# Kernel tuning notes

Measured on AMD Instinct MI355X. Metric: run time of the kernel, lower is better.

The kernel has to match this reference:

```python
import jax, jax.numpy as jnp
import numpy as np

STATE_DIM = 128
ACT_DIM = 32
ENC_K = 10   # encoder_spine_dim
DEC_K = 10   # decoder_dim
H0, H1 = 2048, 2048
BATCH = 16384
MAX_ACTION = 1.0
STD0 = 0.3872983346207417  # sqrt(0.15)


def setup_inputs() -> dict:
    key = jax.random.key(0)
    ks = jax.random.split(key, 10)
    state = jax.random.normal(ks[0], (BATCH, STATE_DIM), dtype=jnp.float32)
    # encoder params: mean linspace over mean_range, std constant
    mean_enc = jnp.broadcast_to(jnp.linspace(-3.0, 3.0, ENC_K, dtype=jnp.float32),
                                (1, STATE_DIM, ENC_K))
    std_enc = jnp.full((1, STATE_DIM, ENC_K), STD0, dtype=jnp.float32)
    def lin(k, fan_in, fan_out):
        bound = 1.0 / np.sqrt(fan_in)
        k1, k2 = jax.random.split(k)
        W = jax.random.uniform(k1, (fan_out, fan_in), jnp.float32, -bound, bound)
        b = jax.random.uniform(k2, (fan_out,), jnp.float32, -bound, bound)
        return W, b
    W1, b1 = lin(ks[1], STATE_DIM * ENC_K, H0)
    W2, b2 = lin(ks[2], H0, H1)
    W3, b3 = lin(ks[3], H1, ACT_DIM * DEC_K)
    # grouped conv1d: weight [act_dim, 1, dec_k], bias [act_dim]
    bound = 1.0 / np.sqrt(DEC_K)
    Wd = jax.random.uniform(ks[4], (ACT_DIM, 1, DEC_K), jnp.float32, -bound, bound)
    bd = jax.random.uniform(ks[5], (ACT_DIM,), jnp.float32, -bound, bound)
    return {"state": state, "mean_enc": mean_enc, "std_enc": std_enc,
            "W1": W1, "b1": b1, "W2": W2, "b2": b2, "W3": W3, "b3": b3,
            "Wd": Wd, "bd": bd}


def reference(state, mean_enc, std_enc, W1, b1, W2, b2, W3, b3, Wd, bd):
    # Population-coding encoder: sigmoid((obs - mean)/std), flattened
    spine = jax.nn.sigmoid((state[:, :, None] - mean_enc) / std_enc)  # [B, D, K]
    spine = spine.reshape(state.shape[0], -1)                         # [B, D*K]
    a = jax.nn.relu(spine @ W1.T + b1)
    a = jax.nn.relu(a @ W2.T + b2)
    a = a @ W3.T + b3                                                 # [B, A*Kd]
    d = a.reshape(-1, ACT_DIM, DEC_K)                                 # [B, A, Kd]
    # grouped Conv1d with kernel == length => per-channel dot product
    raw = jnp.einsum('bak,ak->ba', d, Wd[:, 0, :]) + bd               # [B, A]
    return MAX_ACTION * jnp.tanh(raw)
```

## Files before the change

### kernel.cpp

```cpp
#include <hip/hip_runtime.h>
#include <hip/hip_bf16.h>
#include <stdint.h>

#define BATCH   16384
#define SDIM    128
#define ENCK    10
#define ADIM    32
#define DECK    10
#define HID     2048
#define KSPINE  1280

typedef __bf16 bf16x8 __attribute__((ext_vector_type(8)));
typedef float  f32x4  __attribute__((ext_vector_type(4)));

typedef __attribute__((address_space(1))) const void kGlobalVoid;
typedef __attribute__((address_space(3))) void       kLdsVoid;

__device__ __forceinline__ unsigned short f2b(float f) {
  union { float f; unsigned u; } v; v.f = f;
  unsigned r = v.u + 0x7fffu + ((v.u >> 16) & 1u);
  return (unsigned short)(r >> 16);
}

__global__ void f2b_kernel(const float* __restrict__ in, unsigned* __restrict__ out, int n2) {
  int i = blockIdx.x * blockDim.x + threadIdx.x;
  if (i >= n2) return;
  float2 v = reinterpret_cast<const float2*>(in)[i];
  out[i] = (unsigned)f2b(v.x) | ((unsigned)f2b(v.y) << 16);
}

__global__ void encoder_kernel(const float* __restrict__ state,
                               const float* __restrict__ mean,
                               const float* __restrict__ stdv,
                               unsigned* __restrict__ spine) {
  int idx = blockIdx.x * blockDim.x + threadIdx.x;
  if (idx >= BATCH * SDIM) return;
  int d = idx & (SDIM - 1);
  float x = state[idx];
  float vals[ENCK];
#pragma unroll
  for (int k = 0; k < ENCK; ++k) {
    float z = (x - mean[d * ENCK + k]) / stdv[d * ENCK + k];
    vals[k] = 1.f / (1.f + __expf(-z));
  }
  unsigned* dst = spine + idx * (ENCK / 2);
#pragma unroll
  for (int k = 0; k < ENCK / 2; ++k)
    dst[k] = (unsigned)f2b(vals[2 * k]) | ((unsigned)f2b(vals[2 * k + 1]) << 16);
}

__global__ void weff_kernel(const float* __restrict__ W3, const float* __restrict__ Wd,
                            unsigned short* __restrict__ Weff) {
  int idx = blockIdx.x * 256 + threadIdx.x;
  int a = idx >> 11, j = idx & 2047;
  float s = 0.f;
#pragma unroll
  for (int k = 0; k < DECK; ++k)
    s += Wd[a * DECK + k] * W3[(size_t)(a * DECK + k) * HID + j];
  Weff[idx] = f2b(s);
}

__global__ void beff_kernel(const float* __restrict__ b3, const float* __restrict__ Wd,
                            const float* __restrict__ bd, float* __restrict__ beff) {
  int a = threadIdx.x;
  if (a >= ADIM) return;
  float s = bd[a];
#pragma unroll
  for (int k = 0; k < DECK; ++k) s += Wd[a * DECK + k] * b3[a * DECK + k];
  beff[a] = s;
}


#define A0B 0
#define B0B 32768
#define A1B 65536
#define B1B 98304

#define FENCE asm volatile("" ::: "memory")

#define STAGE(BASEPTR, R0A, R0B, LDS0, LDS1, KT)                                             \
  __builtin_amdgcn_global_load_lds((kGlobalVoid*)((BASEPTR) + (size_t)((R0A) + rs) * K + (KT) + ce), \
                                   (kLdsVoid*)(smem + (LDS0) + t * 16), 16, 0, 0);           \
  __builtin_amdgcn_global_load_lds((kGlobalVoid*)((BASEPTR) + (size_t)((R0B) + rs) * K + (KT) + ce), \
                                   (kLdsVoid*)(smem + (LDS1) + t * 16), 16, 0, 0);

#define DS_AF(DST, ABASE, MPN)                                                               \
  _Pragma("unroll")                                                                          \
  for (int j2 = 0; j2 < 2; ++j2) {                                                           \
    _Pragma("unroll")                                                                        \
    for (int ks = 0; ks < 2; ++ks) {                                                         \
      int rowl = wr * 128 + (MPN) * 32 + j2 * 16 + lr;                                       \
      DST[j2][ks] = *reinterpret_cast<const bf16x8*>(                                        \
          smem + (ABASE) + rowl * 128 + ((((ks) << 6) | (kh << 4)) ^ swz));                  \
    }                                                                                        \
  }

#define DS_B2(DST, NP, BBASE)                                                                \
  _Pragma("unroll")                                                                          \
  for (int ks = 0; ks < 2; ++ks) {                                                           \
    int rowl = wc * 64 + (NP) * 16 + lr;                                                     \
    DST[NP][ks] = *reinterpret_cast<const bf16x8*>(                                          \
        smem + (BBASE) + rowl * 128 + ((((ks) << 6) | (kh << 4)) ^ swz));                    \
  }

#define DS_BF(DST, BBASE)                                                                    \
  _Pragma("unroll")                                                                          \
  for (int n = 0; n < 4; ++n) {                                                              \
    _Pragma("unroll")                                                                        \
    for (int ks = 0; ks < 2; ++ks) {                                                         \
      int rowl = wc * 64 + n * 16 + lr;                                                      \
      DST[n][ks] = *reinterpret_cast<const bf16x8*>(                                         \
          smem + (BBASE) + rowl * 128 + ((((ks) << 6) | (kh << 4)) ^ swz));                  \
    }                                                                                        \
  }

#define MFMA16(MP, AF, BF)                                                                   \
  _Pragma("unroll")                                                                          \
  for (int j2 = 0; j2 < 2; ++j2)                                                             \
    _Pragma("unroll")                                                                        \
    for (int n = 0; n < 4; ++n)                                                              \
      _Pragma("unroll")                                                                      \
      for (int ks = 0; ks < 2; ++ks)                                                         \
        acc[(MP) * 2 + j2][n] = __builtin_amdgcn_mfma_f32_16x16x32_bf16(                     \
            AF[j2][ks], BF[n][ks], acc[(MP) * 2 + j2][n], 0, 0, 0);

#define SGB_PHASE                                                                            \
  __builtin_amdgcn_sched_group_barrier(0x8, 2, 0);                                           \
  __builtin_amdgcn_sched_group_barrier(0x100, 1, 0);                                         \
  __builtin_amdgcn_sched_group_barrier(0x8, 2, 0);                                           \
  __builtin_amdgcn_sched_group_barrier(0x100, 1, 0);                                         \
  __builtin_amdgcn_sched_group_barrier(0x20, 2, 0);                                          \
  __builtin_amdgcn_sched_group_barrier(0x8, 3, 0);                                           \
  __builtin_amdgcn_sched_group_barrier(0x100, 1, 0);                                         \
  __builtin_amdgcn_sched_group_barrier(0x8, 3, 0);                                           \
  __builtin_amdgcn_sched_group_barrier(0x100, 1, 0);                                         \
  __builtin_amdgcn_sched_group_barrier(0x8, 3, 0);                                           \
  __builtin_amdgcn_sched_group_barrier(0x100, 1, 0);                                         \
  __builtin_amdgcn_sched_group_barrier(0x8, 3, 0);                                           \
  __builtin_amdgcn_sched_group_barrier(0x100, 1, 0);

#define VM_NONE
#define VM2 asm volatile("s_waitcnt vmcnt(2)" ::: "memory"); __builtin_amdgcn_sched_barrier(0);
#define VM6 asm volatile("s_waitcnt vmcnt(6)" ::: "memory"); __builtin_amdgcn_sched_barrier(0);

#define PH(MP, AF_C, AF_N, BF_C, BF_N, NXT_A, NXT_MP, BBASE_N, VMW, STG)                     \
  do {                                                                                       \
    asm volatile("s_waitcnt lgkmcnt(0)" ::: "memory");                                       \
    __builtin_amdgcn_sched_barrier(0);                                                       \
    VMW                                                                                      \
    __builtin_amdgcn_s_setprio(1);                                                           \
    MFMA16(MP, AF_C, BF_C);                                                                  \
    __builtin_amdgcn_s_setprio(0);                                                           \
    DS_AF(AF_N, NXT_A, NXT_MP);                                                              \
    DS_B2(BF_N, MP, BBASE_N);                                                                \
    STG;                                                                                     \
    SGB_PHASE;                                                                               \
    FENCE;                                                                                   \
    __builtin_amdgcn_s_barrier();                                                            \
  } while (0)

__global__ __launch_bounds__(512, 2) void gemm256(
    const unsigned short* __restrict__ A,
    const unsigned short* __restrict__ Bw,
    const float* __restrict__ bias,
    unsigned short* __restrict__ Cout,
    int K, int NI) {
  __shared__ char smem[131072];

  const int t    = threadIdx.x;
  const int lane = t & 63;
  const int w    = t >> 6;
  const int wr   = w >> 2;
  const int wc   = w & 3;
  const int lr   = lane & 15;
  const int kh   = lane >> 4;
  const int swz  = (lr & 7) << 4;
  const int rs   = t >> 3;
  const int ce   = ((t & 7) ^ (rs & 7)) << 3;

  const int bid = blockIdx.x;
  const int xcd = bid & 7, idx = bid >> 3;
  const int row0 = (xcd * 8 + (idx >> 3)) * 256;
  const int col0 = (idx & 7) * 256;

  f32x4 acc[8][4];
#pragma unroll
  for (int m = 0; m < 8; ++m)
#pragma unroll
    for (int n = 0; n < 4; ++n)
      acc[m][n] = (f32x4){0.f, 0.f, 0.f, 0.f};

  bf16x8 afc[2][2], afn[2][2], bfA[4][2], bfB[4][2];

  STAGE(Bw, col0 + 0,   col0 + 64,  B0B + 0,     B0B + 8192,  0);
  STAGE(Bw, col0 + 128, col0 + 192, B0B + 16384, B0B + 24576, 0);
  STAGE(A,  row0 + 0,   row0 + 128, A0B + 0,     A0B + 16384, 0);
  STAGE(A,  row0 + 64,  row0 + 192, A0B + 8192,  A0B + 24576, 0);
  STAGE(Bw, col0 + 0,   col0 + 64,  B1B + 0,     B1B + 8192,  64);
  STAGE(Bw, col0 + 128, col0 + 192, B1B + 16384, B1B + 24576, 64);
  STAGE(A,  row0 + 0,   row0 + 128, A1B + 0,     A1B + 16384, 64);
  asm volatile("s_waitcnt vmcnt(0)" ::: "memory");
  FENCE;
  __builtin_amdgcn_s_barrier();
  DS_AF(afc, A0B, 0);
  DS_BF(bfA, B0B);

  for (int i = 0; i < NI; ++i) {
    int kt0 = i << 7;
    int kt1 = kt0 + 64;
    int kt2 = kt0 + 128; if (kt2 >= K) kt2 -= K;
    int kt3 = kt0 + 192; if (kt3 >= K) kt3 -= K;

    PH(0, afc, afn, bfA, bfB, A0B, 1, B1B, VM2,
       STAGE(A,  row0 + 64,  row0 + 192, A1B + 8192,  A1B + 24576, kt1));
    PH(1, afn, afc, bfA, bfB, A0B, 2, B1B, VM_NONE,
       STAGE(Bw, col0 + 0,   col0 + 64,  B0B + 0,     B0B + 8192,  kt2));
    PH(2, afc, afn, bfA, bfB, A0B, 3, B1B, VM_NONE,
       STAGE(Bw, col0 + 128, col0 + 192, B0B + 16384, B0B + 24576, kt2));
    PH(3, afn, afc, bfA, bfB, A1B, 0, B1B, VM6,
       STAGE(A,  row0 + 0,   row0 + 128, A0B + 0,     A0B + 16384, kt2));
    PH(0, afc, afn, bfB, bfA, A1B, 1, B0B, VM2,
       STAGE(A,  row0 + 64,  row0 + 192, A0B + 8192,  A0B + 24576, kt2));
    PH(1, afn, afc, bfB, bfA, A1B, 2, B0B, VM_NONE,
       STAGE(Bw, col0 + 0,   col0 + 64,  B1B + 0,     B1B + 8192,  kt3));
    PH(2, afc, afn, bfB, bfA, A1B, 3, B0B, VM_NONE,
       STAGE(Bw, col0 + 128, col0 + 192, B1B + 16384, B1B + 24576, kt3));
    PH(3, afn, afc, bfB, bfA, A0B, 0, B0B, VM6,
       STAGE(A,  row0 + 0,   row0 + 128, A1B + 0,     A1B + 16384, kt3));
  }

#pragma unroll
  for (int m = 0; m < 8; ++m) {
    int gr0 = row0 + wr * 128 + m * 16 + kh * 4;
#pragma unroll
    for (int n = 0; n < 4; ++n) {
      int gc = col0 + wc * 64 + n * 16 + lr;
      float bv = bias[gc];
#pragma unroll
      for (int v = 0; v < 4; ++v) {
        float val = fmaxf(acc[m][n][v] + bv, 0.f);
        Cout[(size_t)(gr0 + v) * 2048 + gc] = f2b(val);
      }
    }
  }
}

__global__ __launch_bounds__(128) void gemm_skinny(
    const unsigned short* __restrict__ A,
    const unsigned short* __restrict__ Bw,
    const float* __restrict__ beff,
    float* __restrict__ out) {
  const int t = threadIdx.x, lane = t & 63, w = t >> 6;
  const int lr = lane & 15, kh = lane >> 4;
  const int row0 = (blockIdx.x * 2 + w) * 16;
  f32x4 acc[2];
  acc[0] = (f32x4){0.f, 0.f, 0.f, 0.f};
  acc[1] = (f32x4){0.f, 0.f, 0.f, 0.f};

  const unsigned short* Arow = A  + (size_t)(row0 + lr) * HID + kh * 8;
  const unsigned short* B0   = Bw + (size_t)(lr) * HID + kh * 8;
  const unsigned short* B1   = Bw + (size_t)(16 + lr) * HID + kh * 8;

#pragma unroll 4
  for (int kt = 0; kt < HID; kt += 32) {
    bf16x8 a  = *reinterpret_cast<const bf16x8*>(Arow + kt);
    bf16x8 b0 = *reinterpret_cast<const bf16x8*>(B0 + kt);
    bf16x8 b1 = *reinterpret_cast<const bf16x8*>(B1 + kt);
    acc[0] = __builtin_amdgcn_mfma_f32_16x16x32_bf16(a, b0, acc[0], 0, 0, 0);
    acc[1] = __builtin_amdgcn_mfma_f32_16x16x32_bf16(a, b1, acc[1], 0, 0, 0);
  }
#pragma unroll
  for (int n = 0; n < 2; ++n)
#pragma unroll
    for (int v = 0; v < 4; ++v) {
      int row = row0 + kh * 4 + v;
      int col = n * 16 + lr;
      out[(size_t)row * ADIM + col] = tanhf(acc[n][v] + beff[col]);
    }
}

extern "C" void kernel_launch(void* const* d_in, const int* in_sizes, int n_in,
                              void* d_out, int out_size, void* d_ws, size_t ws_size,
                              hipStream_t stream) {
  const float* state    = (const float*)d_in[0];
  const float* mean_enc = (const float*)d_in[1];
  const float* std_enc  = (const float*)d_in[2];
  const float* W1 = (const float*)d_in[3];
  const float* b1 = (const float*)d_in[4];
  const float* W2 = (const float*)d_in[5];
  const float* b2 = (const float*)d_in[6];
  const float* W3 = (const float*)d_in[7];
  const float* b3 = (const float*)d_in[8];
  const float* Wd = (const float*)d_in[9];
  const float* bd = (const float*)d_in[10];

  char* ws = (char*)d_ws;
  unsigned short* W1b   = (unsigned short*)(ws + 0);
  unsigned short* W2b   = (unsigned short*)(ws + 5242880);
  unsigned short* Weff  = (unsigned short*)(ws + 13631488);
  float*          beff  = (float*)(ws + 13762560);
  unsigned short* spine = (unsigned short*)(ws + 13762688);
  unsigned short* h1    = (unsigned short*)(ws + 55705728);
  unsigned short* h2    = (unsigned short*)(ws + 122814592);

  f2b_kernel<<<5120, 256, 0, stream>>>(W1, (unsigned*)W1b, 1310720);
  f2b_kernel<<<8192, 256, 0, stream>>>(W2, (unsigned*)W2b, 2097152);
  weff_kernel<<<256, 256, 0, stream>>>(W3, Wd, Weff);
  beff_kernel<<<1, 64, 0, stream>>>(b3, Wd, bd, beff);

  encoder_kernel<<<(BATCH * SDIM) / 256, 256, 0, stream>>>(state, mean_enc, std_enc, (unsigned*)spine);

  gemm256<<<512, 512, 0, stream>>>(spine, W1b, b1, h1, KSPINE, KSPINE / 128);
  gemm256<<<512, 512, 0, stream>>>(h1,    W2b, b2, h2, HID,    HID / 128);
  gemm_skinny<<<BATCH / 32, 128, 0, stream>>>(h2, Weff, beff, (float*)d_out);
}
```

Before: 249.1 us.

## Split skinny GEMM K across four waves and widen encoder parallelism

The final skinny GEMM now gives each 16-row tile its own block of four waves. Each wave covers a quarter of the K dimension, and the partial results are reduced through shared memory. The encoder is also remapped so each thread writes one packed pair of sigmoid outputs instead of all ten, which spreads the writes over five times as many threads and coalesces the stores. Both changes aim to raise parallelism and memory efficiency in small kernels. They add an LDS reduction, a barrier, and recomputed state loads.

Result: no change. 249.9 us (+0.3%).

```diff
diff --git a/kernel.cpp b/kernel.cpp
--- a/kernel.cpp
+++ b/kernel.cpp
@@ -29,24 +29,21 @@
   out[i] = (unsigned)f2b(v.x) | ((unsigned)f2b(v.y) << 16);
 }
 
-__global__ void encoder_kernel(const float* __restrict__ state,
+__global__ __launch_bounds__(256) void encoder_kernel(const float* __restrict__ state,
                                const float* __restrict__ mean,
                                const float* __restrict__ stdv,
                                unsigned* __restrict__ spine) {
-  int idx = blockIdx.x * blockDim.x + threadIdx.x;
-  if (idx >= BATCH * SDIM) return;
-  int d = idx & (SDIM - 1);
-  float x = state[idx];
-  float vals[ENCK];
-#pragma unroll
-  for (int k = 0; k < ENCK; ++k) {
-    float z = (x - mean[d * ENCK + k]) / stdv[d * ENCK + k];
-    vals[k] = 1.f / (1.f + __expf(-z));
-  }
-  unsigned* dst = spine + idx * (ENCK / 2);
-#pragma unroll
-  for (int k = 0; k < ENCK / 2; ++k)
-    dst[k] = (unsigned)f2b(vals[2 * k]) | ((unsigned)f2b(vals[2 * k + 1]) << 16);
+  int idx = blockIdx.x * 256 + threadIdx.x;
+  int idx1 = (int)(((long long)idx * 0x66666667LL) >> 33);
+  int kk = idx - idx1 * 5;
+  int d  = idx1 & (SDIM - 1);
+  float x = state[idx1];
+  int mi = d * ENCK + kk * 2;
+  float m0 = mean[mi], m1 = mean[mi + 1];
+  float s0 = stdv[mi], s1 = stdv[mi + 1];
+  float v0 = 1.f / (1.f + __expf((m0 - x) / s0));
+  float v1 = 1.f / (1.f + __expf((m1 - x) / s1));
+  spine[idx] = (unsigned)f2b(v0) | ((unsigned)f2b(v1) << 16);
 }
 
 __global__ void weff_kernel(const float* __restrict__ W3, const float* __restrict__ Wd,
@@ -245,38 +242,55 @@
   }
 }
 
-__global__ __launch_bounds__(128) void gemm_skinny(
+__global__ __launch_bounds__(256) void gemm_skinny(
     const unsigned short* __restrict__ A,
     const unsigned short* __restrict__ Bw,
     const float* __restrict__ beff,
     float* __restrict__ out) {
+  __shared__ char red[6144];
   const int t = threadIdx.x, lane = t & 63, w = t >> 6;
   const int lr = lane & 15, kh = lane >> 4;
-  const int row0 = (blockIdx.x * 2 + w) * 16;
+  const int row0 = blockIdx.x * 16;
+  const int kb = w * (HID / 4);
   f32x4 acc[2];
   acc[0] = (f32x4){0.f, 0.f, 0.f, 0.f};
   acc[1] = (f32x4){0.f, 0.f, 0.f, 0.f};
 
-  const unsigned short* Arow = A  + (size_t)(row0 + lr) * HID + kh * 8;
-  const unsigned short* B0   = Bw + (size_t)(lr) * HID + kh * 8;
-  const unsigned short* B1   = Bw + (size_t)(16 + lr) * HID + kh * 8;
+  const unsigned short* Arow = A  + (size_t)(row0 + lr) * HID + kb + kh * 8;
+  const unsigned short* B0   = Bw + (size_t)(lr) * HID + kb + kh * 8;
+  const unsigned short* B1   = Bw + (size_t)(16 + lr) * HID + kb + kh * 8;
 
 #pragma unroll 4
-  for (int kt = 0; kt < HID; kt += 32) {
+  for (int kt = 0; kt < HID / 4; kt += 32) {
     bf16x8 a  = *reinterpret_cast<const bf16x8*>(Arow + kt);
     bf16x8 b0 = *reinterpret_cast<const bf16x8*>(B0 + kt);
     bf16x8 b1 = *reinterpret_cast<const bf16x8*>(B1 + kt);
     acc[0] = __builtin_amdgcn_mfma_f32_16x16x32_bf16(a, b0, acc[0], 0, 0, 0);
     acc[1] = __builtin_amdgcn_mfma_f32_16x16x32_bf16(a, b1, acc[1], 0, 0, 0);
   }
-#pragma unroll
-  for (int n = 0; n < 2; ++n)
-#pragma unroll
-    for (int v = 0; v < 4; ++v) {
-      int row = row0 + kh * 4 + v;
-      int col = n * 16 + lr;
-      out[(size_t)row * ADIM + col] = tanhf(acc[n][v] + beff[col]);
+
+  if (w) {
+    char* p = red + (w - 1) * 2048 + lane * 32;
+    *reinterpret_cast<f32x4*>(p)      = acc[0];
+    *reinterpret_cast<f32x4*>(p + 16) = acc[1];
+  }
+  __syncthreads();
+  if (w == 0) {
+#pragma unroll
+    for (int j = 0; j < 3; ++j) {
+      char* p = red + j * 2048 + lane * 32;
+      acc[0] += *reinterpret_cast<const f32x4*>(p);
+      acc[1] += *reinterpret_cast<const f32x4*>(p + 16);
     }
+#pragma unroll
+    for (int n = 0; n < 2; ++n)
+#pragma unroll
+      for (int v = 0; v < 4; ++v) {
+        int row = row0 + kh * 4 + v;
+        int col = n * 16 + lr;
+        out[(size_t)row * ADIM + col] = tanhf(acc[n][v] + beff[col]);
+      }
+  }
 }
 
 extern "C" void kernel_launch(void* const* d_in, const int* in_sizes, int n_in,
@@ -308,9 +322,9 @@
   weff_kernel<<<256, 256, 0, stream>>>(W3, Wd, Weff);
   beff_kernel<<<1, 64, 0, stream>>>(b3, Wd, bd, beff);
 
-  encoder_kernel<<<(BATCH * SDIM) / 256, 256, 0, stream>>>(state, mean_enc, std_enc, (unsigned*)spine);
+  encoder_kernel<<<(BATCH * SDIM * 5) / 256, 256, 0, stream>>>(state, mean_enc, std_enc, (unsigned*)spine);
 
   gemm256<<<512, 512, 0, stream>>>(spine, W1b, b1, h1, KSPINE, KSPINE / 128);
   gemm256<<<512, 512, 0, stream>>>(h1,    W2b, b2, h2, HID,    HID / 128);
-  gemm_skinny<<<BATCH / 32, 128, 0, stream>>>(h2, Weff, beff, (float*)d_out);
-}
+  gemm_skinny<<<BATCH / 16, 256, 0, stream>>>(h2, Weff, beff, (float*)d_out);
+}
```
